# Performance work log

Hardware: AMD Instinct MI355X
Metric: run time of the kernel (lower is better)

## Reference

```python
import jax, jax.numpy as jnp
import numpy as np

EPS = 1e-12  # torch F.normalize eps

def _colnorm(w, g):
    # F.normalize(w, dim=0, p=2) * g  (column-wise L2 over dim 0)
    n = jnp.sqrt(jnp.sum(w * w, axis=0, keepdims=True))
    return (w / jnp.maximum(n, EPS)) * g

def setup_inputs() -> dict:
    key = jax.random.key(0)
    ks = jax.random.split(key, 16)
    B, T, V, E, H = 16, 512, 8192, 512, 1024
    inp = {
        'xs': jax.random.randint(ks[0], (B, T), 0, V),
        'ys': jax.random.randint(ks[1], (B, T), 0, V),
        'embed_w': jax.random.normal(ks[2], (V, E), jnp.float32) * 0.02,
        'wx': jax.random.normal(ks[3], (E, 4 * H), jnp.float32),
        'wh': jax.random.normal(ks[4], (H, 4 * H), jnp.float32),
        'wmx': jax.random.normal(ks[5], (E, H), jnp.float32),
        'wmh': jax.random.normal(ks[6], (H, H), jnp.float32),
        'b': jax.random.normal(ks[7], (4 * H,), jnp.float32) * 0.02,
        'gx': jax.random.normal(ks[8], (4 * H,), jnp.float32),
        'gh': jax.random.normal(ks[9], (4 * H,), jnp.float32),
        'gmx': jax.random.normal(ks[10], (H,), jnp.float32),
        'gmh': jax.random.normal(ks[11], (H,), jnp.float32),
        'pred_w': jax.random.normal(ks[12], (V, H), jnp.float32) * 0.02,
        'pred_b': jax.random.normal(ks[13], (V,), jnp.float32) * 0.02,
    }
    return inp

def reference(xs, ys, embed_w, wx, wh, wmx, wmh, b, gx, gh, gmx, gmh, pred_w, pred_b):
    B, T = xs.shape
    H = wmh.shape[0]
    V = pred_w.shape[0]
    # padding_idx=0 -> embedding row 0 is zero
    ew = embed_w.at[0].set(0.0)
    x = ew[xs]  # [B, T, E]
    # weight norm
    wx_n = _colnorm(wx, gx)
    wh_n = _colnorm(wh, gh)
    wmx_n = _colnorm(wmx, gmx)
    wmh_n = _colnorm(wmh, gmh)
    # precompute input-dependent projections (same math, batched over time)
    zx = jnp.einsum('bte,ef->btf', x, wx_n) + b     # [B, T, 4H]
    mx = jnp.einsum('bte,eh->bth', x, wmx_n)        # [B, T, H]

    def step(carry, inp):
        h, c = carry
        zx_t, mx_t = inp
        m = mx_t * (h @ wmh_n)                       # [B, H]
        z = zx_t + m @ wh_n                          # [B, 4H]
        i, f, o, u = jnp.split(z, 4, axis=1)
        i = jax.nn.sigmoid(i)
        f = jax.nn.sigmoid(f)
        o = jax.nn.sigmoid(o)
        u = jnp.tanh(u)
        c = f * c + i * u
        h = o * jnp.tanh(c)
        return (h, c), h

    h0 = jnp.zeros((B, H), x.dtype)
    c0 = jnp.zeros((B, H), x.dtype)
    _, hs = jax.lax.scan(step, (h0, c0), (zx.transpose(1, 0, 2), mx.transpose(1, 0, 2)))
    hs = hs.transpose(1, 0, 2)  # [B, T, H]
    logits = jnp.einsum('bth,vh->btv', hs, pred_w) + pred_b
    log_p = jax.nn.log_softmax(logits.reshape(B * T, V), axis=-1)
    nll = -jnp.take_along_axis(log_p, ys.reshape(B * T, 1), axis=1)
    return jnp.mean(nll)
```

## Files before the change

kernel.cpp:

```cpp
#include <hip/hip_runtime.h>
#include <hip/hip_bf16.h>
#include <stdint.h>

#define B_   16
#define T_   512
#define V_   8192
#define E_   512
#define H_   1024
#define BT_  (B_ * T_)
#define H4_  (4 * H_)

typedef __attribute__((ext_vector_type(8))) short   short8;
typedef __attribute__((ext_vector_type(8))) __bf16  bf16x8;
typedef __attribute__((ext_vector_type(4))) float   f32x4;
typedef __attribute__((ext_vector_type(4))) short   short4v;
typedef unsigned long long ull;

__device__ __forceinline__ float bf2f(short s) {
  union { unsigned u; float f; } x;
  x.u = ((unsigned)(unsigned short)s) << 16;
  return x.f;
}
__device__ __forceinline__ short f2bf(float f) {
  union { float f; unsigned u; } x; x.f = f;
  unsigned u = x.u;
  u = (u + 0x7fffu + ((u >> 16) & 1u)) >> 16;
  return (short)u;
}
__device__ __forceinline__ f32x4 mfma16(short8 a, short8 b, f32x4 c) {
  return __builtin_amdgcn_mfma_f32_16x16x32_bf16(
      __builtin_bit_cast(bf16x8, a), __builtin_bit_cast(bf16x8, b), c, 0, 0, 0);
}
__device__ __forceinline__ float sigm(float x) { return 1.f / (1.f + __expf(-x)); }
__device__ __forceinline__ float tanh_f(float x) { return 1.f - 2.f / (__expf(2.f * x) + 1.f); }

__device__ __forceinline__ short8 mk8(ull lo, ull hi) {
  union { ull u[2]; short8 s; } c;
  c.u[0] = lo; c.u[1] = hi;
  return c.s;
}

__global__ __launch_bounds__(256) void colscale(const float* __restrict__ W,
                                                const float* __restrict__ g,
                                                float* __restrict__ sc, int Kr, int N) {
  int j = blockIdx.x * 256 + threadIdx.x;
  if (j >= N) return;
  float ss = 0.f;
  for (int i = 0; i < Kr; ++i) { float v = W[(long)i * N + j]; ss = fmaf(v, v, ss); }
  sc[j] = g[j] / fmaxf(sqrtf(ss), 1e-12f);
}

__global__ __launch_bounds__(256) void transpose_cast(const float* __restrict__ W,
                                                      const float* __restrict__ sc,
                                                      short* __restrict__ WT, int Kr, int N) {
  __shared__ float tile[32][33];
  int nbi = Kr >> 5;
  int bi = blockIdx.x % nbi, bj = blockIdx.x / nbi;
  int i0 = bi << 5, j0 = bj << 5;
  int tx = threadIdx.x & 31, ty = threadIdx.x >> 5;
  for (int yy = ty; yy < 32; yy += 8)
    tile[yy][tx] = W[(long)(i0 + yy) * N + j0 + tx];
  __syncthreads();
  for (int yy = ty; yy < 32; yy += 8) {
    int j = j0 + yy;
    WT[(long)j * Kr + i0 + tx] = f2bf(tile[tx][yy] * sc[j]);
  }
}

__global__ __launch_bounds__(256) void castbf(const float* __restrict__ src,
                                              short* __restrict__ dst, long n) {
  long i = ((long)blockIdx.x * 256 + threadIdx.x) * 4;
  if (i + 3 < n) {
    float4 v = *(const float4*)(src + i);
    short4v o = { f2bf(v.x), f2bf(v.y), f2bf(v.z), f2bf(v.w) };
    *(short4v*)(dst + i) = o;
  }
}

__global__ __launch_bounds__(256) void embed_gather(const int* __restrict__ xs,
                                                    const float* __restrict__ ew,
                                                    short* __restrict__ x) {
  int r = blockIdx.x;
  int idx = xs[r];
  const float* src = ew + (long)idx * E_;
  for (int e = threadIdx.x; e < E_; e += 256) {
    float v = (idx == 0) ? 0.f : src[e];
    x[(long)r * E_ + e] = f2bf(v);
  }
}

__global__ __launch_bounds__(256) void gemm_bt(const short* __restrict__ A,
                                               const short* __restrict__ BT,
                                               const float* __restrict__ bias,
                                               short* __restrict__ C,
                                               int M, int N, int K) {
  int ntiles = N >> 7;
  int tM = (blockIdx.x / ntiles) << 7;
  int tN = (blockIdx.x % ntiles) << 7;
  int w = threadIdx.x >> 6, lane = threadIdx.x & 63;
  int mo = tM + ((w & 1) << 6), no = tN + ((w >> 1) << 6);
  int lr = lane & 15, lk8 = (lane >> 4) << 3, q = lane >> 4;
  f32x4 acc[4][4] = {};
  const short* Ap = A + (long)(mo + lr) * K + lk8;
  const short* Bp = BT + (long)(no + lr) * K + lk8;
  for (int k0 = 0; k0 < K; k0 += 32) {
    short8 af[4], bfr[4];
#pragma unroll
    for (int i = 0; i < 4; ++i) af[i] = *(const short8*)(Ap + (long)16 * i * K + k0);
#pragma unroll
    for (int j = 0; j < 4; ++j) bfr[j] = *(const short8*)(Bp + (long)16 * j * K + k0);
#pragma unroll
    for (int i = 0; i < 4; ++i)
#pragma unroll
      for (int j = 0; j < 4; ++j)
        acc[i][j] = mfma16(af[i], bfr[j], acc[i][j]);
  }
  float pbv[4];
#pragma unroll
  for (int j = 0; j < 4; ++j) pbv[j] = bias ? bias[no + 16 * j + lr] : 0.f;
#pragma unroll
  for (int i = 0; i < 4; ++i)
#pragma unroll
    for (int j = 0; j < 4; ++j)
#pragma unroll
      for (int r = 0; r < 4; ++r) {
        int row = mo + 16 * i + 4 * q + r;
        int col = no + 16 * j + lr;
        C[(long)row * N + col] = f2bf(acc[i][j][r] + pbv[j]);
      }
}

__global__ __launch_bounds__(256) void gemm_logits(const short* __restrict__ A,
                                                   const short* __restrict__ BT,
                                                   const float* __restrict__ pb,
                                                   const int* __restrict__ ys,
                                                   float* __restrict__ sumexp,
                                                   float* __restrict__ logit_y,
                                                   int M, int N, int K) {
  int ntiles = N >> 7;
  int tM = (blockIdx.x / ntiles) << 7;
  int tN = (blockIdx.x % ntiles) << 7;
  int w = threadIdx.x >> 6, lane = threadIdx.x & 63;
  int mo = tM + ((w & 1) << 6), no = tN + ((w >> 1) << 6);
  int lr = lane & 15, lk8 = (lane >> 4) << 3, q = lane >> 4;
  f32x4 acc[4][4] = {};
  const short* Ap = A + (long)(mo + lr) * K + lk8;
  const short* Bp = BT + (long)(no + lr) * K + lk8;
  for (int k0 = 0; k0 < K; k0 += 32) {
    short8 af[4], bfr[4];
#pragma unroll
    for (int i = 0; i < 4; ++i) af[i] = *(const short8*)(Ap + (long)16 * i * K + k0);
#pragma unroll
    for (int j = 0; j < 4; ++j) bfr[j] = *(const short8*)(Bp + (long)16 * j * K + k0);
#pragma unroll
    for (int i = 0; i < 4; ++i)
#pragma unroll
      for (int j = 0; j < 4; ++j)
        acc[i][j] = mfma16(af[i], bfr[j], acc[i][j]);
  }
  float pbv[4];
#pragma unroll
  for (int j = 0; j < 4; ++j) pbv[j] = pb[no + 16 * j + lr];
#pragma unroll
  for (int i = 0; i < 4; ++i) {
#pragma unroll
    for (int r = 0; r < 4; ++r) {
      int row = mo + 16 * i + 4 * q + r;
      int ysr = ys[row];
      float s = 0.f;
#pragma unroll
      for (int j = 0; j < 4; ++j) {
        float v = acc[i][j][r] + pbv[j];
        s += __expf(v);
        int col = no + 16 * j + lr;
        if (col == ysr) logit_y[row] = v;
      }
      s += __shfl_xor(s, 1); s += __shfl_xor(s, 2);
      s += __shfl_xor(s, 4); s += __shfl_xor(s, 8);
      if (lr == 0) atomicAdd(&sumexp[row], s);
    }
  }
}

#define NWG_ 64

__global__ __launch_bounds__(256, 1) void scan_kernel(
    const short* __restrict__ zxb, const short* __restrict__ mxb,
    const short* __restrict__ wmhT, const short* __restrict__ whT,
    short* __restrict__ hs,
    ull* __restrict__ h_prev,
    ull* __restrict__ m_buf,
    unsigned* __restrict__ flags_m,
    unsigned* __restrict__ flags_h) {
  const int g = blockIdx.x;
  const int tid = threadIdx.x;
  const int w = tid >> 6, lane = tid & 63;
  const int lr = lane & 15, q = lane >> 4;
  const int colg = g << 4;
  const int b = tid >> 4, cl = tid & 15;

  __shared__ float red1[4][16][16];
  __shared__ float red2[4][4][16][16];
  __shared__ __align__(8) short mtile[16][16];
  __shared__ __align__(8) short htile[16][16];

  short8 wmh_f[8];
#pragma unroll
  for (int kk = 0; kk < 8; ++kk) {
    const ull* p = (const ull*)(wmhT + (long)(colg + lr) * H_ + (w << 8) + (kk << 5) + (q << 3));
    ull lo = __hip_atomic_load(p, __ATOMIC_RELAXED, __HIP_MEMORY_SCOPE_WORKGROUP);
    ull hi = __hip_atomic_load(p + 1, __ATOMIC_RELAXED, __HIP_MEMORY_SCOPE_WORKGROUP);
    wmh_f[kk] = mk8(lo, hi);
  }
  short8 wh_f[4][8];
#pragma unroll
  for (int gt = 0; gt < 4; ++gt)
#pragma unroll
    for (int kk = 0; kk < 8; ++kk) {
      const ull* p = (const ull*)(whT + (long)(gt * H_ + colg + lr) * H_ + (w << 8) + (kk << 5) + (q << 3));
      ull lo = __hip_atomic_load(p, __ATOMIC_RELAXED, __HIP_MEMORY_SCOPE_WORKGROUP);
      ull hi = __hip_atomic_load(p + 1, __ATOMIC_RELAXED, __HIP_MEMORY_SCOPE_WORKGROUP);
      wh_f[gt][kk] = mk8(lo, hi);
    }

  float c = 0.f;
  const ull* hp = h_prev + lr * 256 + (w << 6) + (q << 1);
  const ull* mp = m_buf + lr * 256 + (w << 6) + (q << 1);

  for (int t = 0; t < T_; ++t) {
    long rrow = (long)(b * T_ + t);
    short mx_p = mxb[rrow * H_ + colg + cl];
    const short* zrow = zxb + rrow * H4_ + colg + cl;
    short z0p = zrow[0 * H_], z1p = zrow[1 * H_], z2p = zrow[2 * H_], z3p = zrow[3 * H_];

    if (tid < NWG_)
      while (__hip_atomic_load(&flags_h[tid << 5], __ATOMIC_RELAXED,
                               __HIP_MEMORY_SCOPE_AGENT) < (unsigned)t) {}
    __syncthreads();

    ull lh[16];
#pragma unroll
    for (int kk = 0; kk < 8; ++kk) {
      lh[2 * kk]     = __hip_atomic_load(hp + (kk << 3),     __ATOMIC_RELAXED, __HIP_MEMORY_SCOPE_AGENT);
      lh[2 * kk + 1] = __hip_atomic_load(hp + (kk << 3) + 1, __ATOMIC_RELAXED, __HIP_MEMORY_SCOPE_AGENT);
    }
    f32x4 a1 = {};
#pragma unroll
    for (int kk = 0; kk < 8; ++kk)
      a1 = mfma16(mk8(lh[2 * kk], lh[2 * kk + 1]), wmh_f[kk], a1);
#pragma unroll
    for (int r = 0; r < 4; ++r) red1[w][q * 4 + r][lr] = a1[r];
    __syncthreads();
    {
      float hw = red1[0][b][cl] + red1[1][b][cl] + red1[2][b][cl] + red1[3][b][cl];
      mtile[b][cl] = f2bf(bf2f(mx_p) * hw);
    }
    __syncthreads();
    if (tid < 64) {
      int b2 = tid >> 2, ch = tid & 3;
      ull v = *(const ull*)&mtile[b2][ch << 2];
      __hip_atomic_store(&m_buf[b2 * 256 + (colg >> 2) + ch], v,
                         __ATOMIC_RELAXED, __HIP_MEMORY_SCOPE_AGENT);
      __builtin_amdgcn_s_waitcnt(0);
      if (tid == 0)
        __hip_atomic_store(&flags_m[g << 5], (unsigned)(t + 1),
                           __ATOMIC_RELAXED, __HIP_MEMORY_SCOPE_AGENT);
    }

    if (tid < NWG_)
      while (__hip_atomic_load(&flags_m[tid << 5], __ATOMIC_RELAXED,
                               __HIP_MEMORY_SCOPE_AGENT) < (unsigned)(t + 1)) {}
    __syncthreads();

    ull lm[16];
#pragma unroll
    for (int kk = 0; kk < 8; ++kk) {
      lm[2 * kk]     = __hip_atomic_load(mp + (kk << 3),     __ATOMIC_RELAXED, __HIP_MEMORY_SCOPE_AGENT);
      lm[2 * kk + 1] = __hip_atomic_load(mp + (kk << 3) + 1, __ATOMIC_RELAXED, __HIP_MEMORY_SCOPE_AGENT);
    }
    f32x4 a2[4] = {};
#pragma unroll
    for (int kk = 0; kk < 8; ++kk) {
      short8 mf = mk8(lm[2 * kk], lm[2 * kk + 1]);
#pragma unroll
      for (int gt = 0; gt < 4; ++gt)
        a2[gt] = mfma16(mf, wh_f[gt][kk], a2[gt]);
    }
#pragma unroll
    for (int gt = 0; gt < 4; ++gt)
#pragma unroll
      for (int r = 0; r < 4; ++r)
        red2[w][gt][q * 4 + r][lr] = a2[gt][r];
    __syncthreads();
    {
      float zi = red2[0][0][b][cl] + red2[1][0][b][cl] + red2[2][0][b][cl] + red2[3][0][b][cl] + bf2f(z0p);
      float zf = red2[0][1][b][cl] + red2[1][1][b][cl] + red2[2][1][b][cl] + red2[3][1][b][cl] + bf2f(z1p);
      float zo = red2[0][2][b][cl] + red2[1][2][b][cl] + red2[2][2][b][cl] + red2[3][2][b][cl] + bf2f(z2p);
      float zu = red2[0][3][b][cl] + red2[1][3][b][cl] + red2[2][3][b][cl] + red2[3][3][b][cl] + bf2f(z3p);
      float ig = sigm(zi), fg = sigm(zf), og = sigm(zo), ug = tanh_f(zu);
      c = fg * c + ig * ug;
      float h = og * tanh_f(c);
      short hb = f2bf(h);
      htile[b][cl] = hb;
      hs[rrow * H_ + colg + cl] = hb;
    }
    __syncthreads();
    if (tid < 64) {
      int b2 = tid >> 2, ch = tid & 3;
      ull v = *(const ull*)&htile[b2][ch << 2];
      __hip_atomic_store(&h_prev[b2 * 256 + (colg >> 2) + ch], v,
                         __ATOMIC_RELAXED, __HIP_MEMORY_SCOPE_AGENT);
      __builtin_amdgcn_s_waitcnt(0);
      if (tid == 0)
        __hip_atomic_store(&flags_h[g << 5], (unsigned)(t + 1),
                           __ATOMIC_RELAXED, __HIP_MEMORY_SCOPE_AGENT);
    }
  }
}

__global__ __launch_bounds__(256) void reduce_nll(const float* __restrict__ se,
                                                  const float* __restrict__ ly,
                                                  float* __restrict__ out) {
  __shared__ float buf[256];
  float s = 0.f;
  for (int r = threadIdx.x; r < BT_; r += 256)
    s += logf(se[r]) - ly[r];
  buf[threadIdx.x] = s;
  __syncthreads();
  for (int off = 128; off > 0; off >>= 1) {
    if (threadIdx.x < off) buf[threadIdx.x] += buf[threadIdx.x + off];
    __syncthreads();
  }
  if (threadIdx.x == 0) out[0] = buf[0] * (1.0f / BT_);
}

extern "C" void kernel_launch(void* const* d_in, const int* in_sizes, int n_in,
                              void* d_out, int out_size, void* d_ws, size_t ws_size,
                              hipStream_t stream) {
  const int*   xs     = (const int*)d_in[0];
  const int*   ys     = (const int*)d_in[1];
  const float* embw   = (const float*)d_in[2];
  const float* wx     = (const float*)d_in[3];
  const float* wh     = (const float*)d_in[4];
  const float* wmx    = (const float*)d_in[5];
  const float* wmh    = (const float*)d_in[6];
  const float* bias   = (const float*)d_in[7];
  const float* gx     = (const float*)d_in[8];
  const float* gh     = (const float*)d_in[9];
  const float* gmx    = (const float*)d_in[10];
  const float* gmh    = (const float*)d_in[11];
  const float* pred_w = (const float*)d_in[12];
  const float* pred_b = (const float*)d_in[13];
  float* out = (float*)d_out;

  char* base = (char*)d_ws;
  size_t off = 0;
  auto alloc = [&](size_t bytes) -> void* {
    void* p = base + off;
    off = (off + bytes + 255) & ~(size_t)255;
    return p;
  };
  short* xb     = (short*)alloc((size_t)BT_ * E_ * 2);
  short* zxb    = (short*)alloc((size_t)BT_ * H4_ * 2);
  short* mxb    = (short*)alloc((size_t)BT_ * H_ * 2);
  short* hs     = (short*)alloc((size_t)BT_ * H_ * 2);
  short* wxT    = (short*)alloc((size_t)H4_ * E_ * 2);
  short* whT    = (short*)alloc((size_t)H4_ * H_ * 2);
  short* wmxT   = (short*)alloc((size_t)H_ * E_ * 2);
  short* wmhT   = (short*)alloc((size_t)H_ * H_ * 2);
  short* pwb    = (short*)alloc((size_t)V_ * H_ * 2);
  float* scx    = (float*)alloc(H4_ * 4);
  float* sch    = (float*)alloc(H4_ * 4);
  float* scmx   = (float*)alloc(H_ * 4);
  float* scmh   = (float*)alloc(H_ * 4);
  float* l_y    = (float*)alloc(BT_ * 4);
  ull*   m_buf  = (ull*)alloc(B_ * H_ * 2);
  size_t z0 = off;
  float*    sumexp  = (float*)alloc(BT_ * 4);
  unsigned* flags_m = (unsigned*)alloc(NWG_ * 32 * 4);
  unsigned* flags_h = (unsigned*)alloc(NWG_ * 32 * 4);
  ull*      h_prev  = (ull*)alloc(B_ * H_ * 2);
  size_t zlen = off - z0;

  hipMemsetAsync(base + z0, 0, zlen, stream);

  colscale<<<H4_ / 256, 256, 0, stream>>>(wx, gx, scx, E_, H4_);
  colscale<<<H4_ / 256, 256, 0, stream>>>(wh, gh, sch, H_, H4_);
  colscale<<<H_ / 256, 256, 0, stream>>>(wmx, gmx, scmx, E_, H_);
  colscale<<<H_ / 256, 256, 0, stream>>>(wmh, gmh, scmh, H_, H_);
  transpose_cast<<<(E_ / 32) * (H4_ / 32), 256, 0, stream>>>(wx, scx, wxT, E_, H4_);
  transpose_cast<<<(H_ / 32) * (H4_ / 32), 256, 0, stream>>>(wh, sch, whT, H_, H4_);
  transpose_cast<<<(E_ / 32) * (H_ / 32), 256, 0, stream>>>(wmx, scmx, wmxT, E_, H_);
  transpose_cast<<<(H_ / 32) * (H_ / 32), 256, 0, stream>>>(wmh, scmh, wmhT, H_, H_);
  castbf<<<((long)V_ * H_) / 1024, 256, 0, stream>>>(pred_w, pwb, (long)V_ * H_);

  embed_gather<<<BT_, 256, 0, stream>>>(xs, embw, xb);
  gemm_bt<<<(BT_ / 128) * (H4_ / 128), 256, 0, stream>>>(xb, wxT, bias, zxb, BT_, H4_, E_);
  gemm_bt<<<(BT_ / 128) * (H_ / 128), 256, 0, stream>>>(xb, wmxT, nullptr, mxb, BT_, H_, E_);

  scan_kernel<<<NWG_, 256, 0, stream>>>(zxb, mxb, wmhT, whT, hs,
                                        h_prev, m_buf, flags_m, flags_h);

  gemm_logits<<<(BT_ / 128) * (V_ / 128), 256, 0, stream>>>(hs, pwb, pred_b, ys,
                                                            sumexp, l_y, BT_, V_, H_);
  reduce_nll<<<1, 256, 0, stream>>>(sumexp, l_y, out);
}
```

Baseline: 5.774 ms.

## Embed step tags in exchanged data to drop flags; stage logits GEMM via LDS

```diff
diff --git a/kernel.cpp b/kernel.cpp
--- a/kernel.cpp
+++ b/kernel.cpp
@@ -38,6 +38,21 @@
   union { ull u[2]; short8 s; } c;
   c.u[0] = lo; c.u[1] = hi;
   return c.s;
+}
+__device__ __forceinline__ short8 pk8(ull a, ull b, ull c, ull d) {
+  union { unsigned u[4]; short8 s; } x;
+  x.u[0] = (unsigned)a; x.u[1] = (unsigned)b;
+  x.u[2] = (unsigned)c; x.u[3] = (unsigned)d;
+  return x.s;
+}
+__device__ __forceinline__ ull packv(short v0, short v1, unsigned ep) {
+  return (ull)(unsigned short)v0 | ((ull)(unsigned short)v1 << 16) | ((ull)ep << 32);
+}
+
+__device__ __forceinline__ void gload_lds16(const short* g, short* l) {
+  __builtin_amdgcn_global_load_lds(
+      (const __attribute__((address_space(1))) unsigned int*)g,
+      (__attribute__((address_space(3))) unsigned int*)l, 16, 0, 0);
 }
 
 __global__ __launch_bounds__(256) void colscale(const float* __restrict__ W,
@@ -137,42 +152,59 @@
                                                    float* __restrict__ sumexp,
                                                    float* __restrict__ logit_y,
                                                    int M, int N, int K) {
+  __shared__ short As[128 * 32];
+  __shared__ short Bs[128 * 32];
   int ntiles = N >> 7;
   int tM = (blockIdx.x / ntiles) << 7;
   int tN = (blockIdx.x % ntiles) << 7;
   int w = threadIdx.x >> 6, lane = threadIdx.x & 63;
-  int mo = tM + ((w & 1) << 6), no = tN + ((w >> 1) << 6);
-  int lr = lane & 15, lk8 = (lane >> 4) << 3, q = lane >> 4;
+  int mo = (w & 1) << 6, no = (w >> 1) << 6;
+  int lr = lane & 15, q = lane >> 4;
+  int sr = lane >> 2, sk = (lane & 3) << 3;
   f32x4 acc[4][4] = {};
-  const short* Ap = A + (long)(mo + lr) * K + lk8;
-  const short* Bp = BT + (long)(no + lr) * K + lk8;
+
+  const short* Ag = A + (long)(tM + 32 * w + sr) * K + sk;
+  const short* Bg = BT + (long)(tN + 32 * w + sr) * K + sk;
+  short* Al0 = As + (32 * w) * 32;
+  short* Al1 = As + (32 * w + 16) * 32;
+  short* Bl0 = Bs + (32 * w) * 32;
+  short* Bl1 = Bs + (32 * w + 16) * 32;
+
   for (int k0 = 0; k0 < K; k0 += 32) {
+    gload_lds16(Ag + k0, Al0);
+    gload_lds16(Ag + k0 + (long)16 * K, Al1);
+    gload_lds16(Bg + k0, Bl0);
+    gload_lds16(Bg + k0 + (long)16 * K, Bl1);
+    __syncthreads();
     short8 af[4], bfr[4];
 #pragma unroll
-    for (int i = 0; i < 4; ++i) af[i] = *(const short8*)(Ap + (long)16 * i * K + k0);
-#pragma unroll
-    for (int j = 0; j < 4; ++j) bfr[j] = *(const short8*)(Bp + (long)16 * j * K + k0);
+    for (int i = 0; i < 4; ++i) af[i] = *(const short8*)(As + (mo + 16 * i + lr) * 32 + q * 8);
+#pragma unroll
+    for (int j = 0; j < 4; ++j) bfr[j] = *(const short8*)(Bs + (no + 16 * j + lr) * 32 + q * 8);
 #pragma unroll
     for (int i = 0; i < 4; ++i)
 #pragma unroll
       for (int j = 0; j < 4; ++j)
         acc[i][j] = mfma16(af[i], bfr[j], acc[i][j]);
-  }
+    __syncthreads();
+  }
+
+  int moG = tM + mo, noG = tN + no;
   float pbv[4];
 #pragma unroll
-  for (int j = 0; j < 4; ++j) pbv[j] = pb[no + 16 * j + lr];
+  for (int j = 0; j < 4; ++j) pbv[j] = pb[noG + 16 * j + lr];
 #pragma unroll
   for (int i = 0; i < 4; ++i) {
 #pragma unroll
     for (int r = 0; r < 4; ++r) {
-      int row = mo + 16 * i + 4 * q + r;
+      int row = moG + 16 * i + 4 * q + r;
       int ysr = ys[row];
       float s = 0.f;
 #pragma unroll
       for (int j = 0; j < 4; ++j) {
         float v = acc[i][j][r] + pbv[j];
         s += __expf(v);
-        int col = no + 16 * j + lr;
+        int col = noG + 16 * j + lr;
         if (col == ysr) logit_y[row] = v;
       }
       s += __shfl_xor(s, 1); s += __shfl_xor(s, 2);
@@ -188,10 +220,8 @@
     const short* __restrict__ zxb, const short* __restrict__ mxb,
     const short* __restrict__ wmhT, const short* __restrict__ whT,
     short* __restrict__ hs,
-    ull* __restrict__ h_prev,
-    ull* __restrict__ m_buf,
-    unsigned* __restrict__ flags_m,
-    unsigned* __restrict__ flags_h) {
+    ull* __restrict__ h_pack,
+    ull* __restrict__ m_pack) {
   const int g = blockIdx.x;
   const int tid = threadIdx.x;
   const int w = tid >> 6, lane = tid & 63;
@@ -224,8 +254,11 @@
     }
 
   float c = 0.f;
-  const ull* hp = h_prev + lr * 256 + (w << 6) + (q << 1);
-  const ull* mp = m_buf + lr * 256 + (w << 6) + (q << 1);
+  const ull* hb = h_pack + lr * 512 + (w << 7) + (q << 2);
+  const ull* mb = m_pack + lr * 512 + (w << 7) + (q << 2);
+  const int pb2 = tid >> 3, pj = tid & 7;
+  ull* mst = m_pack + pb2 * 512 + (colg >> 1) + pj;
+  ull* hst = h_pack + pb2 * 512 + (colg >> 1) + pj;
 
   for (int t = 0; t < T_; ++t) {
     long rrow = (long)(b * T_ + t);
@@ -233,21 +266,27 @@
     const short* zrow = zxb + rrow * H4_ + colg + cl;
     short z0p = zrow[0 * H_], z1p = zrow[1 * H_], z2p = zrow[2 * H_], z3p = zrow[3 * H_];
 
-    if (tid < NWG_)
-      while (__hip_atomic_load(&flags_h[tid << 5], __ATOMIC_RELAXED,
-                               __HIP_MEMORY_SCOPE_AGENT) < (unsigned)t) {}
-    __syncthreads();
-
-    ull lh[16];
-#pragma unroll
-    for (int kk = 0; kk < 8; ++kk) {
-      lh[2 * kk]     = __hip_atomic_load(hp + (kk << 3),     __ATOMIC_RELAXED, __HIP_MEMORY_SCOPE_AGENT);
-      lh[2 * kk + 1] = __hip_atomic_load(hp + (kk << 3) + 1, __ATOMIC_RELAXED, __HIP_MEMORY_SCOPE_AGENT);
+    ull hv[32];
+    {
+      const unsigned et = (unsigned)t;
+      for (;;) {
+        unsigned bad = 0;
+#pragma unroll
+        for (int kk = 0; kk < 8; ++kk)
+#pragma unroll
+          for (int u = 0; u < 4; ++u)
+            hv[kk * 4 + u] = __hip_atomic_load(hb + (kk << 4) + u,
+                                               __ATOMIC_RELAXED, __HIP_MEMORY_SCOPE_AGENT);
+#pragma unroll
+        for (int i = 0; i < 32; ++i) bad |= ((unsigned)(hv[i] >> 32)) ^ et;
+        if (__all(bad == 0)) break;
+      }
     }
     f32x4 a1 = {};
 #pragma unroll
     for (int kk = 0; kk < 8; ++kk)
-      a1 = mfma16(mk8(lh[2 * kk], lh[2 * kk + 1]), wmh_f[kk], a1);
+      a1 = mfma16(pk8(hv[4 * kk], hv[4 * kk + 1], hv[4 * kk + 2], hv[4 * kk + 3]),
+                  wmh_f[kk], a1);
 #pragma unroll
     for (int r = 0; r < 4; ++r) red1[w][q * 4 + r][lr] = a1[r];
     __syncthreads();
@@ -256,32 +295,31 @@
       mtile[b][cl] = f2bf(bf2f(mx_p) * hw);
     }
     __syncthreads();
-    if (tid < 64) {
-      int b2 = tid >> 2, ch = tid & 3;
-      ull v = *(const ull*)&mtile[b2][ch << 2];
-      __hip_atomic_store(&m_buf[b2 * 256 + (colg >> 2) + ch], v,
-                         __ATOMIC_RELAXED, __HIP_MEMORY_SCOPE_AGENT);
-      __builtin_amdgcn_s_waitcnt(0);
-      if (tid == 0)
-        __hip_atomic_store(&flags_m[g << 5], (unsigned)(t + 1),
-                           __ATOMIC_RELAXED, __HIP_MEMORY_SCOPE_AGENT);
-    }
-
-    if (tid < NWG_)
-      while (__hip_atomic_load(&flags_m[tid << 5], __ATOMIC_RELAXED,
-                               __HIP_MEMORY_SCOPE_AGENT) < (unsigned)(t + 1)) {}
-    __syncthreads();
-
-    ull lm[16];
+    if (tid < 128) {
+      ull v = packv(mtile[pb2][2 * pj], mtile[pb2][2 * pj + 1], (unsigned)(t + 1));
+      __hip_atomic_store(mst, v, __ATOMIC_RELAXED, __HIP_MEMORY_SCOPE_AGENT);
+    }
+
+    ull lm[32];
+    {
+      const unsigned et = (unsigned)(t + 1);
+      for (;;) {
+        unsigned bad = 0;
+#pragma unroll
+        for (int kk = 0; kk < 8; ++kk)
+#pragma unroll
+          for (int u = 0; u < 4; ++u)
+            lm[kk * 4 + u] = __hip_atomic_load(mb + (kk << 4) + u,
+                                               __ATOMIC_RELAXED, __HIP_MEMORY_SCOPE_AGENT);
+#pragma unroll
+        for (int i = 0; i < 32; ++i) bad |= ((unsigned)(lm[i] >> 32)) ^ et;
+        if (__all(bad == 0)) break;
+      }
+    }
+    f32x4 a2[4] = {};
 #pragma unroll
     for (int kk = 0; kk < 8; ++kk) {
-      lm[2 * kk]     = __hip_atomic_load(mp + (kk << 3),     __ATOMIC_RELAXED, __HIP_MEMORY_SCOPE_AGENT);
-      lm[2 * kk + 1] = __hip_atomic_load(mp + (kk << 3) + 1, __ATOMIC_RELAXED, __HIP_MEMORY_SCOPE_AGENT);
-    }
-    f32x4 a2[4] = {};
-#pragma unroll
-    for (int kk = 0; kk < 8; ++kk) {
-      short8 mf = mk8(lm[2 * kk], lm[2 * kk + 1]);
+      short8 mf = pk8(lm[4 * kk], lm[4 * kk + 1], lm[4 * kk + 2], lm[4 * kk + 3]);
 #pragma unroll
       for (int gt = 0; gt < 4; ++gt)
         a2[gt] = mfma16(mf, wh_f[gt][kk], a2[gt]);
@@ -300,20 +338,14 @@
       float ig = sigm(zi), fg = sigm(zf), og = sigm(zo), ug = tanh_f(zu);
       c = fg * c + ig * ug;
       float h = og * tanh_f(c);
-      short hb = f2bf(h);
-      htile[b][cl] = hb;
-      hs[rrow * H_ + colg + cl] = hb;
-    }
-    __syncthreads();
-    if (tid < 64) {
-      int b2 = tid >> 2, ch = tid & 3;
-      ull v = *(const ull*)&htile[b2][ch << 2];
-      __hip_atomic_store(&h_prev[b2 * 256 + (colg >> 2) + ch], v,
-                         __ATOMIC_RELAXED, __HIP_MEMORY_SCOPE_AGENT);
-      __builtin_amdgcn_s_waitcnt(0);
-      if (tid == 0)
-        __hip_atomic_store(&flags_h[g << 5], (unsigned)(t + 1),
-                           __ATOMIC_RELAXED, __HIP_MEMORY_SCOPE_AGENT);
+      short hb16 = f2bf(h);
+      htile[b][cl] = hb16;
+      hs[rrow * H_ + colg + cl] = hb16;
+    }
+    __syncthreads();
+    if (tid < 128) {
+      ull v = packv(htile[pb2][2 * pj], htile[pb2][2 * pj + 1], (unsigned)(t + 1));
+      __hip_atomic_store(hst, v, __ATOMIC_RELAXED, __HIP_MEMORY_SCOPE_AGENT);
     }
   }
 }
@@ -374,12 +406,10 @@
   float* scmx   = (float*)alloc(H_ * 4);
   float* scmh   = (float*)alloc(H_ * 4);
   float* l_y    = (float*)alloc(BT_ * 4);
-  ull*   m_buf  = (ull*)alloc(B_ * H_ * 2);
   size_t z0 = off;
-  float*    sumexp  = (float*)alloc(BT_ * 4);
-  unsigned* flags_m = (unsigned*)alloc(NWG_ * 32 * 4);
-  unsigned* flags_h = (unsigned*)alloc(NWG_ * 32 * 4);
-  ull*      h_prev  = (ull*)alloc(B_ * H_ * 2);
+  float* sumexp = (float*)alloc(BT_ * 4);
+  ull*   h_pack = (ull*)alloc((size_t)B_ * 512 * 8);
+  ull*   m_pack = (ull*)alloc((size_t)B_ * 512 * 8);
   size_t zlen = off - z0;
 
   hipMemsetAsync(base + z0, 0, zlen, stream);
@@ -398,8 +428,7 @@
   gemm_bt<<<(BT_ / 128) * (H4_ / 128), 256, 0, stream>>>(xb, wxT, bias, zxb, BT_, H4_, E_);
   gemm_bt<<<(BT_ / 128) * (H_ / 128), 256, 0, stream>>>(xb, wmxT, nullptr, mxb, BT_, H_, E_);
 
-  scan_kernel<<<NWG_, 256, 0, stream>>>(zxb, mxb, wmhT, whT, hs,
-                                        h_prev, m_buf, flags_m, flags_h);
+  scan_kernel<<<NWG_, 256, 0, stream>>>(zxb, mxb, wmhT, whT, hs, h_pack, m_pack);
 
   gemm_logits<<<(BT_ / 128) * (V_ / 128), 256, 0, stream>>>(hs, pwb, pred_b, ys,
                                                             sumexp, l_y, BT_, V_, H_);
```

New measurement: 8.388 ms. 1.45x slower.
